# Kernel optimization log

Measured on AMD Instinct MI355X. Metric: run time of the kernel, lower is better.

The kernel has to match this reference:

```python
import jax, jax.numpy as jnp
import numpy as np

HIDDEN = 2048
N_HEADS = 16
HEAD_DIM = 128
N_KV_HEADS = 4
MAX_POS = 4096
NEG_INF = -1e9


def _fixed_pos_embedding(features, length):
    # matches generate_fixed_pos_embedding: freqs over arange(0, features, 2)/features
    fraction = jnp.arange(0, features, 2, dtype=jnp.float32) / features
    timescale = 10000.0 ** fraction
    inv_freq = 1.0 / timescale
    sinusoid = jnp.einsum('i,j->ij', jnp.arange(length, dtype=jnp.float32), inv_freq)
    sinusoid = jnp.concatenate([sinusoid, sinusoid], axis=-1)  # [length, features]
    return jnp.sin(sinusoid), jnp.cos(sinusoid)


def setup_inputs() -> dict:
    key = jax.random.key(0)
    k0, k1, k2, k3, k4 = jax.random.split(key, 5)
    B, S = 2, 2048
    hidden_states = jax.random.normal(k0, (B, S, HIDDEN), dtype=jnp.float32)
    # causal additive mask [B,1,S,S]; module forces mask[:, :, :, 0] = 0
    causal = jnp.where(jnp.tril(jnp.ones((S, S), dtype=bool)), 0.0, NEG_INF).astype(jnp.float32)
    causal = causal.at[:, 0].set(0.0)
    attention_mask = jnp.broadcast_to(causal[None, None], (B, 1, S, S))
    std = 0.02
    q_w = jax.random.normal(k1, (N_HEADS * HEAD_DIM, HIDDEN), dtype=jnp.float32) * std
    k_w = jax.random.normal(k2, (N_KV_HEADS * HEAD_DIM, HIDDEN), dtype=jnp.float32) * std
    v_w = jax.random.normal(k3, (N_KV_HEADS * HEAD_DIM, HIDDEN), dtype=jnp.float32) * std
    o_w = jax.random.normal(k4, (HIDDEN, N_HEADS * HEAD_DIM), dtype=jnp.float32) * std
    sin, cos = _fixed_pos_embedding(HEAD_DIM, MAX_POS)
    return {"hidden_states": hidden_states, "attention_mask": attention_mask,
            "q_w": q_w, "k_w": k_w, "v_w": v_w, "o_w": o_w, "sin": sin, "cos": cos}


def _rotate_half(x):
    d = x.shape[-1] // 2
    return jnp.concatenate([-x[..., d:], x[..., :d]], axis=-1)


def reference(hidden_states, attention_mask, q_w, k_w, v_w, o_w, sin, cos):
    B, S, _ = hidden_states.shape
    D = cos.shape[-1]
    H = q_w.shape[0] // D
    KV = k_w.shape[0] // D
    n_rep = H // KV

    # QKV projections (nn.Linear: y = x @ W^T), split into heads: [B,S,h,D]
    q = jnp.einsum('bsh,oh->bso', hidden_states, q_w).reshape(B, S, H, D)
    k = jnp.einsum('bsh,oh->bso', hidden_states, k_w).reshape(B, S, KV, D)
    v = jnp.einsum('bsh,oh->bso', hidden_states, v_w).reshape(B, S, KV, D)

    # rotary embedding (non-decode path: q and k share cos/sin[:S])
    c = cos[:S][None, :, None, :]
    s = sin[:S][None, :, None, :]
    q = q * c + _rotate_half(q) * s
    k = k * c + _rotate_half(k) * s

    # repeat_kv (repeat_interleave along head dim) for GQA
    k = jnp.repeat(k, n_rep, axis=2)  # [B,S,H,D]
    v = jnp.repeat(v, n_rep, axis=2)

    # NOTE: no 1/sqrt(D) scaling -- module uses softmax_scale=1.0
    scores = jnp.einsum('bqhd,bkhd->bhqk', q, k) + attention_mask
    weights = jax.nn.softmax(scores.astype(jnp.float32), axis=-1).astype(q.dtype)
    attn = jnp.einsum('bhqk,bkhd->bqhd', weights, v).reshape(B, S, H * D)
    return jnp.einsum('bso,ho->bsh', attn, o_w)
```

## Files before the change

### kernel.cpp

```cpp
#include <hip/hip_runtime.h>

typedef __bf16 bf16x8 __attribute__((ext_vector_type(8)));
typedef float f32x4 __attribute__((ext_vector_type(4)));

#define LOG2E 1.44269504088896340736f

#define GLDS16(g, l) __builtin_amdgcn_global_load_lds(                         \
    (const __attribute__((address_space(1))) unsigned int*)(g),                \
    (__attribute__((address_space(3))) unsigned int*)(l), 16, 0, 0)


__global__ __launch_bounds__(256) void megasplit(
    const float* __restrict__ hs, const float* __restrict__ qw,
    const float* __restrict__ kw, const float* __restrict__ vw,
    const float* __restrict__ ow,
    __bf16* __restrict__ hsh, __bf16* __restrict__ hsl,
    __bf16* __restrict__ wqh, __bf16* __restrict__ wql,
    __bf16* __restrict__ owh, __bf16* __restrict__ owl)
{
    int bid = blockIdx.x;
    const float* src; __bf16* dh; __bf16* dl;
    if (bid < 4096)      { src = hs; dh = hsh; dl = hsl; }
    else if (bid < 6144) { bid -= 4096; src = qw; dh = wqh; dl = wql; }
    else if (bid < 6656) { bid -= 6144; src = kw;
                           dh = wqh + (size_t)2048 * 2048;
                           dl = wql + (size_t)2048 * 2048; }
    else if (bid < 7168) { bid -= 6656; src = vw;
                           dh = wqh + (size_t)2560 * 2048;
                           dl = wql + (size_t)2560 * 2048; }
    else                 { bid -= 7168; src = ow; dh = owh; dl = owl; }

    const size_t t = (size_t)(bid * 256 + threadIdx.x) * 8;
    float4 a = *(const float4*)(src + t);
    float4 b = *(const float4*)(src + t + 4);
    float f[8] = {a.x, a.y, a.z, a.w, b.x, b.y, b.z, b.w};
    bf16x8 h, l;
#pragma unroll
    for (int i = 0; i < 8; ++i) {
        __bf16 hh = (__bf16)f[i];
        h[i] = hh; l[i] = (__bf16)(f[i] - (float)hh);
    }
    const int r  = (int)(t >> 11);
    const int sw = (r ^ (r >> 2)) & 3;
    const size_t d = (t & ~(size_t)31) + ((size_t)((((int)(t >> 3) & 3) ^ sw)) << 3);
    *(bf16x8*)(dh + d) = h;
    *(bf16x8*)(dl + d) = l;
}

template<int BN, int NLOAD>
__global__ __launch_bounds__(512, 2) void gemm_planes8(
    const __bf16* __restrict__ Ah, const __bf16* __restrict__ Al,
    const __bf16* __restrict__ Bh, const __bf16* __restrict__ Bl,
    float* __restrict__ C, int ldc)
{
    constexpr int WN = BN / 4;
    constexpr int NF = WN / 16;

    __shared__ __bf16 sAh[2][256 * 32];
    __shared__ __bf16 sAl[2][256 * 32];
    __shared__ __bf16 sBh[2][BN * 32];
    __shared__ __bf16 sBl[2][BN * 32];

    const int tid  = threadIdx.x;
    const int lane = tid & 63;
    const int wave = tid >> 6;
    const int wm   = (wave & 1) * 128;
    const int wn   = (wave >> 1) * WN;

    const int idg = blockIdx.y * 16 + blockIdx.x;
    const int swb = (idg & 7) * 32 + (idg >> 3);
    const int m0  = (swb >> 4) * 256;
    const int n0  = (swb & 15) * BN;

    const int fr  = lane & 15;
    const int g   = lane >> 4;
    const int dr  = g * 4;
    const int sxr = (fr ^ (fr >> 2)) & 3;
    const int pA  = (g ^ sxr) << 3;

    const int srow = tid >> 2;
    const int spb  = (tid & 3) << 3;
    const __bf16* gAh0 = Ah + (size_t)(m0 + srow) * 2048 + spb;
    const __bf16* gAh1 = gAh0 + (size_t)128 * 2048;
    const __bf16* gAl0 = Al + (size_t)(m0 + srow) * 2048 + spb;
    const __bf16* gAl1 = gAl0 + (size_t)128 * 2048;
    const __bf16* gBh0 = Bh + (size_t)(n0 + srow) * 2048 + spb;
    const __bf16* gBl0 = Bl + (size_t)(n0 + srow) * 2048 + spb;
    const __bf16* gX5  = Bl;
    const __bf16* gBl6 = Bl;
    if constexpr (BN == 192) {
        gX5 = (tid < 256)
            ? Bh + (size_t)(n0 + 128 + srow) * 2048 + spb
            : Bl + (size_t)(n0 + ((tid - 256) >> 2)) * 2048 + (((tid - 256) & 3) << 3);
        gBl6 = Bl + (size_t)(n0 + 64 + srow) * 2048 + spb;
    }

#define STAGE8(bb)                                                             \
    do {                                                                       \
        GLDS16(gAh0, &sAh[bb][tid * 8]);                                       \
        GLDS16(gAh1, &sAh[bb][4096 + tid * 8]);                                \
        GLDS16(gAl0, &sAl[bb][tid * 8]);                                       \
        GLDS16(gAl1, &sAl[bb][4096 + tid * 8]);                                \
        GLDS16(gBh0, &sBh[bb][tid * 8]);                                       \
        if constexpr (BN == 192) {                                             \
            if (tid < 256) { GLDS16(gX5, &sBh[bb][4096 + tid * 8]); }          \
            else           { GLDS16(gX5, &sBl[bb][(tid - 256) * 8]); }         \
            GLDS16(gBl6, &sBl[bb][2048 + tid * 8]);                            \
        } else {                                                               \
            GLDS16(gBl0, &sBl[bb][tid * 8]);                                   \
        }                                                                      \
    } while (0)

#define ADV8()                                                                 \
    do {                                                                       \
        gAh0 += 32; gAh1 += 32; gAl0 += 32; gAl1 += 32;                        \
        gBh0 += 32; gBl0 += 32;                                                \
        if constexpr (BN == 192) { gX5 += 32; gBl6 += 32; }                    \
    } while (0)

    f32x4 acc[8][NF];
#pragma unroll
    for (int mf = 0; mf < 8; ++mf)
#pragma unroll
        for (int nf = 0; nf < NF; ++nf)
            acc[mf][nf] = (f32x4){0.f, 0.f, 0.f, 0.f};

    STAGE8(0);
    ADV8();

    for (int t = 0; t < 64; ++t) {
        const int buf = t & 1;

        __builtin_amdgcn_sched_barrier(0);
        asm volatile("s_waitcnt vmcnt(0)" ::: "memory");
        __builtin_amdgcn_sched_barrier(0);
        __builtin_amdgcn_s_barrier();
        __builtin_amdgcn_sched_barrier(0);
        if (t < 63) {
            STAGE8(buf ^ 1);
            ADV8();
        }
        __builtin_amdgcn_sched_barrier(0);

        bf16x8 bh[NF], bl[NF];
#pragma unroll
        for (int nf = 0; nf < NF; ++nf) {
            bh[nf] = *(const bf16x8*)&sBh[buf][(wn + nf * 16 + fr) * 32 + pA];
            bl[nf] = *(const bf16x8*)&sBl[buf][(wn + nf * 16 + fr) * 32 + pA];
        }
        __builtin_amdgcn_s_setprio(1);
#pragma unroll
        for (int p = 0; p < 4; ++p) {
            bf16x8 a0h = *(const bf16x8*)&sAh[buf][(wm + p * 32 + fr) * 32 + pA];
            bf16x8 a0l = *(const bf16x8*)&sAl[buf][(wm + p * 32 + fr) * 32 + pA];
            bf16x8 a1h = *(const bf16x8*)&sAh[buf][(wm + p * 32 + 16 + fr) * 32 + pA];
            bf16x8 a1l = *(const bf16x8*)&sAl[buf][(wm + p * 32 + 16 + fr) * 32 + pA];
#pragma unroll
            for (int nf = 0; nf < NF; ++nf) {
                acc[2 * p][nf] = __builtin_amdgcn_mfma_f32_16x16x32_bf16(a0h, bh[nf], acc[2 * p][nf], 0, 0, 0);
                acc[2 * p][nf] = __builtin_amdgcn_mfma_f32_16x16x32_bf16(a0l, bh[nf], acc[2 * p][nf], 0, 0, 0);
                acc[2 * p][nf] = __builtin_amdgcn_mfma_f32_16x16x32_bf16(a0h, bl[nf], acc[2 * p][nf], 0, 0, 0);
                acc[2 * p + 1][nf] = __builtin_amdgcn_mfma_f32_16x16x32_bf16(a1h, bh[nf], acc[2 * p + 1][nf], 0, 0, 0);
                acc[2 * p + 1][nf] = __builtin_amdgcn_mfma_f32_16x16x32_bf16(a1l, bh[nf], acc[2 * p + 1][nf], 0, 0, 0);
                acc[2 * p + 1][nf] = __builtin_amdgcn_mfma_f32_16x16x32_bf16(a1h, bl[nf], acc[2 * p + 1][nf], 0, 0, 0);
            }
        }
        __builtin_amdgcn_s_setprio(0);
    }

#pragma unroll
    for (int mf = 0; mf < 8; ++mf)
#pragma unroll
        for (int nf = 0; nf < NF; ++nf)
#pragma unroll
            for (int rr = 0; rr < 4; ++rr) {
                const int row = m0 + wm + mf * 16 + dr + rr;
                const int col = n0 + wn + nf * 16 + fr;
                C[(size_t)row * ldc + col] = acc[mf][nf][rr];
            }
#undef STAGE8
#undef ADV8
}

__global__ __launch_bounds__(256) void rope_prep(
    float* __restrict__ qkv,
    const float* __restrict__ sinp, const float* __restrict__ cosp,
    __bf16* __restrict__ ksp, __bf16* __restrict__ vtsp)
{
    __shared__ float vs[32][132];
    const int tid = threadIdx.x;

    if (blockIdx.x < 16384) {
        int t = blockIdx.x * 256 + tid;
        int row = t >> 10;
        int rem = t & 1023;
        int col = (rem >> 6) * 128 + (rem & 63);
        int s = row & 2047;
        int d = col & 127;

        float* p = qkv + (size_t)row * 3072 + col;
        float x0  = p[0];
        float x1  = p[64];
        float c0  = cosp[s * 128 + d];
        float c1  = cosp[s * 128 + d + 64];
        float sn0 = sinp[s * 128 + d];
        float sn1 = sinp[s * 128 + d + 64];
        p[0]  = x0 * c0 - x1 * sn0;
        p[64] = x1 * c1 + x0 * sn1;
        return;
    }

    const int pidx = blockIdx.x - 16384;
    const int kb  = pidx & 15;
    const int kvh = (pidx >> 4) & 3;
    const int b   = pidx >> 6;

    {
        const int key = tid >> 1;
        const int dh  = (tid & 1) * 32;
        const int pos = kb * 128 + key;
        const int ksw = key & 7;
        const float* src = qkv + (size_t)(b * 2048 + pos) * 3072 + 2048 + kvh * 128;
        __bf16* dst = ksp + ((size_t)((b * 4 + kvh) * 2048) + pos) * 256;
        const float* cp = cosp + pos * 128;
        const float* sp = sinp + pos * 128;
#pragma unroll
        for (int g = 0; g < 4; ++g) {
            int d0 = dh + g * 8;
            float4 x0a = *(const float4*)(src + d0);
            float4 x0b = *(const float4*)(src + d0 + 4);
            float4 x1a = *(const float4*)(src + d0 + 64);
            float4 x1b = *(const float4*)(src + d0 + 68);
            float4 c0a = *(const float4*)(cp + d0);
            float4 c0b = *(const float4*)(cp + d0 + 4);
            float4 c1a = *(const float4*)(cp + d0 + 64);
            float4 c1b = *(const float4*)(cp + d0 + 68);
            float4 s0a = *(const float4*)(sp + d0);
            float4 s0b = *(const float4*)(sp + d0 + 4);
            float4 s1a = *(const float4*)(sp + d0 + 64);
            float4 s1b = *(const float4*)(sp + d0 + 68);
            float x0[8] = {x0a.x,x0a.y,x0a.z,x0a.w,x0b.x,x0b.y,x0b.z,x0b.w};
            float x1[8] = {x1a.x,x1a.y,x1a.z,x1a.w,x1b.x,x1b.y,x1b.z,x1b.w};
            float c0[8] = {c0a.x,c0a.y,c0a.z,c0a.w,c0b.x,c0b.y,c0b.z,c0b.w};
            float c1[8] = {c1a.x,c1a.y,c1a.z,c1a.w,c1b.x,c1b.y,c1b.z,c1b.w};
            float s0[8] = {s0a.x,s0a.y,s0a.z,s0a.w,s0b.x,s0b.y,s0b.z,s0b.w};
            float s1[8] = {s1a.x,s1a.y,s1a.z,s1a.w,s1b.x,s1b.y,s1b.z,s1b.w};
            bf16x8 h0, l0, h1, l1;
#pragma unroll
            for (int i = 0; i < 8; ++i) {
                float y0 = x0[i] * c0[i] - x1[i] * s0[i];
                float y1 = x1[i] * c1[i] + x0[i] * s1[i];
                __bf16 hh0 = (__bf16)y0;
                __bf16 hh1 = (__bf16)y1;
                h0[i] = hh0; l0[i] = (__bf16)(y0 - (float)hh0);
                h1[i] = hh1; l1[i] = (__bf16)(y1 - (float)hh1);
            }
            const int bb = d0 >> 3;
            *(bf16x8*)(dst + ((bb        ^ ksw) << 3)) = h0;
            *(bf16x8*)(dst + (((bb + 8)  ^ ksw) << 3)) = h1;
            *(bf16x8*)(dst + (((bb + 16) ^ ksw) << 3)) = l0;
            *(bf16x8*)(dst + (((bb + 24) ^ ksw) << 3)) = l1;
        }
    }

    for (int st = 0; st < 4; ++st) {
        __syncthreads();
        {
            const int key = tid >> 3;
            const int dc  = (tid & 7) * 16;
            const float* vsrc = qkv + (size_t)(b * 2048 + kb * 128 + st * 32 + key) * 3072
                                + 2560 + kvh * 128 + dc;
            float4 v0 = *(const float4*)(vsrc);
            float4 v1 = *(const float4*)(vsrc + 4);
            float4 v2 = *(const float4*)(vsrc + 8);
            float4 v3 = *(const float4*)(vsrc + 12);
            *(float4*)&vs[key][dc]      = v0;
            *(float4*)&vs[key][dc + 4]  = v1;
            *(float4*)&vs[key][dc + 8]  = v2;
            *(float4*)&vs[key][dc + 12] = v3;
        }
        __syncthreads();
        {
            const int plane = tid >> 7;
            const int d     = tid & 127;
            bf16x8 ob[4];
#pragma unroll
            for (int k = 0; k < 32; ++k) {
                float x = vs[k][d];
                __bf16 hh = (__bf16)x;
                ob[k >> 3][k & 7] = plane ? (__bf16)(x - (float)hh) : hh;
            }
            const int rV  = plane * 128 + d;
            const int vsw = (d >> 1) & 3;
            __bf16* dst = vtsp + ((size_t)((b * 4 + kvh) * 64 + kb * 4 + st)) * 8192
                               + (size_t)rV * 32;
            *(bf16x8*)(dst + ((0 ^ vsw) << 3)) = ob[0];
            *(bf16x8*)(dst + ((1 ^ vsw) << 3)) = ob[1];
            *(bf16x8*)(dst + ((2 ^ vsw) << 3)) = ob[2];
            *(bf16x8*)(dst + ((3 ^ vsw) << 3)) = ob[3];
        }
    }
}

__global__ __launch_bounds__(512, 4) void flash_attn(
    const float* __restrict__ qkv,
    const __bf16* __restrict__ ksp,
    const __bf16* __restrict__ vtsp,
    __bf16* __restrict__ attnh, __bf16* __restrict__ attnl)
{
    __shared__ __bf16 Ks[2][32 * 256];
    __shared__ __bf16 Vt[2][256 * 32];
    __shared__ unsigned int Psf[4][2][512];

    const int tid  = threadIdx.x;
    const int lane = tid & 63;
    const int wave = tid >> 6;
    const int hw   = wave & 3;
    const int rs   = wave >> 2;
    const int id   = blockIdx.x;
    const int pair = id & 7;
    const int kvh  = pair & 3;
    const int b    = pair >> 2;
    const int u    = id >> 3;
    const int qb   = (u >> 5) ? (u & 31) : 63 - (u & 31);
    const int h    = kvh * 4 + hw;

    const int fr  = lane & 15;
    const int g   = lane >> 4;
    const int fc  = g * 8;
    const int dr  = g * 4;
    const int frs = fr & 7;

    bf16x8 aqh[4], aql[4];
    {
        const size_t qrow = (size_t)(b * 2048 + qb * 32 + rs * 16 + fr) * 3072 + h * 128;
#pragma unroll
        for (int ks = 0; ks < 4; ++ks) {
            float4 qv[2];
            qv[0] = *(const float4*)(qkv + qrow + ks * 32 + fc);
            qv[1] = *(const float4*)(qkv + qrow + ks * 32 + fc + 4);
            const float* qf = (const float*)qv;
            bf16x8 h8, l8;
#pragma unroll
            for (int i = 0; i < 8; ++i) {
                float x = qf[i];
                __bf16 hh = (__bf16)x;
                h8[i] = hh; l8[i] = (__bf16)(x - (float)hh);
            }
            aqh[ks] = h8; aql[ks] = l8;
        }
    }
    asm volatile("s_waitcnt vmcnt(0)" ::: "memory");
    __builtin_amdgcn_sched_barrier(0);

    bf16x8 ones;
#pragma unroll
    for (int i = 0; i < 8; ++i) ones[i] = (__bf16)1.0f;

    f32x4 o[8];
#pragma unroll
    for (int dg = 0; dg < 8; ++dg) o[dg] = (f32x4){0.f, 0.f, 0.f, 0.f};
    f32x4 ls = (f32x4){0.f, 0.f, 0.f, 0.f};

    const int ntiles = qb + 1;
    const __bf16* kg0 = ksp + (size_t)(b * 4 + kvh) * 2048 * 256 + wave * 1024 + lane * 8;
    const __bf16* vg0 = vtsp + (size_t)(b * 4 + kvh) * 64 * 8192 + wave * 1024 + lane * 8;

    {
        __bf16* kl = &Ks[0][wave * 1024];
        __bf16* vl = &Vt[0][wave * 1024];
        GLDS16(kg0, kl); GLDS16(kg0 + 512, kl + 512);
        GLDS16(vg0, vl); GLDS16(vg0 + 512, vl + 512);
    }

    for (int kt = 0; kt < ntiles; ++kt) {
        if (kt + 1 < ntiles) {
            const __bf16* kg = kg0 + (size_t)(kt + 1) * 8192;
            const __bf16* vg = vg0 + (size_t)(kt + 1) * 8192;
            __bf16* kl = &Ks[(kt + 1) & 1][wave * 1024];
            __bf16* vl = &Vt[(kt + 1) & 1][wave * 1024];
            GLDS16(kg, kl); GLDS16(kg + 512, kl + 512);
            GLDS16(vg, vl); GLDS16(vg + 512, vl + 512);
            asm volatile("s_waitcnt vmcnt(4)" ::: "memory");
        } else {
            asm volatile("s_waitcnt vmcnt(0)" ::: "memory");
        }
        __builtin_amdgcn_sched_barrier(0);
        __builtin_amdgcn_s_barrier();
        __builtin_amdgcn_sched_barrier(0);

        const int buf = kt & 1;
        const int k0 = kt * 32;

        f32x4 s0v = (f32x4){0.f, 0.f, 0.f, 0.f};
        f32x4 s1v = (f32x4){0.f, 0.f, 0.f, 0.f};
        __builtin_amdgcn_s_setprio(1);
#pragma unroll
        for (int ks = 0; ks < 4; ++ks) {
            const int bh = ks * 4 + g;
            bf16x8 b0h = *(const bf16x8*)&Ks[buf][fr * 256        + ((bh        ^ frs) << 3)];
            bf16x8 b0l = *(const bf16x8*)&Ks[buf][fr * 256        + (((bh + 16) ^ frs) << 3)];
            bf16x8 b1h = *(const bf16x8*)&Ks[buf][(16 + fr) * 256 + ((bh        ^ frs) << 3)];
            bf16x8 b1l = *(const bf16x8*)&Ks[buf][(16 + fr) * 256 + (((bh + 16) ^ frs) << 3)];
            s0v = __builtin_amdgcn_mfma_f32_16x16x32_bf16(aqh[ks], b0h, s0v, 0, 0, 0);
            s0v = __builtin_amdgcn_mfma_f32_16x16x32_bf16(aql[ks], b0h, s0v, 0, 0, 0);
            s0v = __builtin_amdgcn_mfma_f32_16x16x32_bf16(aqh[ks], b0l, s0v, 0, 0, 0);
            s1v = __builtin_amdgcn_mfma_f32_16x16x32_bf16(aqh[ks], b1h, s1v, 0, 0, 0);
            s1v = __builtin_amdgcn_mfma_f32_16x16x32_bf16(aql[ks], b1h, s1v, 0, 0, 0);
            s1v = __builtin_amdgcn_mfma_f32_16x16x32_bf16(aqh[ks], b1l, s1v, 0, 0, 0);
        }
        __builtin_amdgcn_s_setprio(0);

        if (kt == ntiles - 1) {
#pragma unroll
            for (int r = 0; r < 4; ++r) {
                const int qg = qb * 32 + rs * 16 + dr + r;
                if (k0 + fr > qg)      s0v[r] = -1e30f;
                if (k0 + 16 + fr > qg) s1v[r] = -1e30f;
            }
        }
        {
            uint4 w0, w1;
#pragma unroll
            for (int r = 0; r < 4; ++r) {
                float x0 = exp2f(s0v[r] * LOG2E);
                float x1 = exp2f(s1v[r] * LOG2E);
                __bf16 h0 = (__bf16)x0;
                __bf16 h1 = (__bf16)x1;
                unsigned u0 = ((unsigned)__builtin_bit_cast(unsigned short, h0) << 16)
                            |  (unsigned)__builtin_bit_cast(unsigned short, (__bf16)(x0 - (float)h0));
                unsigned u1 = ((unsigned)__builtin_bit_cast(unsigned short, h1) << 16)
                            |  (unsigned)__builtin_bit_cast(unsigned short, (__bf16)(x1 - (float)h1));
                ((unsigned*)&w0)[r] = u0;
                ((unsigned*)&w1)[r] = u1;
            }
            unsigned int* pw = &Psf[hw][rs][0];
            const int sb = (fr * 4 + g) ^ (((fr >> 3) & 1) << 2);
            *(uint4*)(pw + sb * 4)        = w0;
            *(uint4*)(pw + (sb + 64) * 4) = w1;
        }
        asm volatile("s_waitcnt lgkmcnt(0)" ::: "memory");
        __builtin_amdgcn_sched_barrier(0);

        bf16x8 ph, pl;
#pragma unroll
        for (int j = 0; j < 8; ++j) {
            const int col = fc + j;
            const int sR  = (col * 4 + (fr >> 2)) ^ ((g & 1) << 2);
            const unsigned v = Psf[hw][rs][sR * 4 + (fr & 3)];
            ph[j] = __builtin_bit_cast(__bf16, (unsigned short)(v >> 16));
            pl[j] = __builtin_bit_cast(__bf16, (unsigned short)(v & 0xffffu));
        }

        __builtin_amdgcn_s_setprio(1);
        ls = __builtin_amdgcn_mfma_f32_16x16x32_bf16(ph, ones, ls, 0, 0, 0);
        ls = __builtin_amdgcn_mfma_f32_16x16x32_bf16(pl, ones, ls, 0, 0, 0);
#pragma unroll
        for (int dg = 0; dg < 8; ++dg) {
            const int d0 = dg * 16 + fr;
            const int sw = (g ^ ((d0 >> 1) & 3)) << 3;
            bf16x8 bvh = *(const bf16x8*)&Vt[buf][d0 * 32 + sw];
            bf16x8 bvl = *(const bf16x8*)&Vt[buf][(d0 + 128) * 32 + sw];
            o[dg] = __builtin_amdgcn_mfma_f32_16x16x32_bf16(ph, bvh, o[dg], 0, 0, 0);
            o[dg] = __builtin_amdgcn_mfma_f32_16x16x32_bf16(pl, bvh, o[dg], 0, 0, 0);
            o[dg] = __builtin_amdgcn_mfma_f32_16x16x32_bf16(ph, bvl, o[dg], 0, 0, 0);
        }
        __builtin_amdgcn_s_setprio(0);

        __builtin_amdgcn_s_barrier();
    }

    {
        const size_t orow = (size_t)(b * 2048 + qb * 32 + rs * 16);
#pragma unroll
        for (int dg = 0; dg < 8; ++dg)
#pragma unroll
            for (int r = 0; r < 4; ++r) {
                float val = o[dg][r] / ls[r];
                const int rl  = dr + r;
                const int swz = (rl ^ (rl >> 2)) & 3;
                const int col = h * 128 + dg * 16 + fr;
                const size_t idx = (size_t)(orow + rl) * 2048 + (col & ~31)
                                 + ((((col >> 3) & 3) ^ swz) << 3) + (col & 7);
                __bf16 hh = (__bf16)val;
                attnh[idx] = hh;
                attnl[idx] = (__bf16)(val - (float)hh);
            }
    }
}

extern "C" void kernel_launch(void* const* d_in, const int* in_sizes, int n_in,
                              void* d_out, int out_size, void* d_ws, size_t ws_size,
                              hipStream_t stream)
{
    const float* hs   = (const float*)d_in[0];
    const float* qw   = (const float*)d_in[2];
    const float* kw   = (const float*)d_in[3];
    const float* vw   = (const float*)d_in[4];
    const float* ow   = (const float*)d_in[5];
    const float* sinp = (const float*)d_in[6];
    const float* cosp = (const float*)d_in[7];
    float* outp = (float*)d_out;

    char* w = (char*)d_ws;
    float*  qkv  = (float*)w;   w += (size_t)4096 * 3072 * 4;
    __bf16* ksp  = (__bf16*)w;  w += (size_t)8 * 2048 * 256 * 2;
    __bf16* vtsp = (__bf16*)w;  w += (size_t)8 * 64 * 8192 * 2;
    __bf16* wqh  = (__bf16*)w;  w += (size_t)3072 * 2048 * 2;
    __bf16* wql  = (__bf16*)w;  w += (size_t)3072 * 2048 * 2;
    __bf16* owh  = (__bf16*)w;  w += (size_t)2048 * 2048 * 2;
    __bf16* owl  = (__bf16*)w;  w += (size_t)2048 * 2048 * 2;
    __bf16* hsh  = (__bf16*)w;  w += (size_t)4096 * 2048 * 2;
    __bf16* hsl  = (__bf16*)w;  w += (size_t)4096 * 2048 * 2;
    __bf16* attnh = hsh;
    __bf16* attnl = hsl;

    megasplit<<<9216, 256, 0, stream>>>(hs, qw, kw, vw, ow,
                                        hsh, hsl, wqh, wql, owh, owl);
    gemm_planes8<192, 7><<<dim3(16, 16), 512, 0, stream>>>(hsh, hsl, wqh, wql, qkv, 3072);
    rope_prep<<<16512, 256, 0, stream>>>(qkv, sinp, cosp, ksp, vtsp);
    flash_attn<<<512, 512, 0, stream>>>(qkv, ksp, vtsp, attnh, attnl);
    gemm_planes8<128, 6><<<dim3(16, 16), 512, 0, stream>>>(attnh, attnl, owh, owl, outp, 2048);
}
```

Measured before the change: 578.5 us.

## Switch split-bf16 GEMMs to 32x32x16 MFMA with 4x2 wave tiling

Rewrites the split-precision GEMM inner loop to use 32x32x16 bf16 MFMA instructions instead of 16x16x32, and rearranges waves into a 4x2 grid of 64-row by BN/2-column tiles. Each wave now loads larger fragments per k-half and issues fewer, larger MFMAs, which is meant to cut LDS read traffic per FLOP and raise matrix-core throughput. The accumulator layout and output store indexing change to match the 32x32 fragment layout, which risks slower or less coalesced stores and higher register pressure.

```diff
diff --git a/kernel.cpp b/kernel.cpp
--- a/kernel.cpp
+++ b/kernel.cpp
@@ -2,6 +2,7 @@
 
 typedef __bf16 bf16x8 __attribute__((ext_vector_type(8)));
 typedef float f32x4 __attribute__((ext_vector_type(4)));
+typedef float f32x16 __attribute__((ext_vector_type(16)));
 
 #define LOG2E 1.44269504088896340736f
 
@@ -48,13 +49,14 @@
 }
 
 template<int BN, int NLOAD>
-__global__ __launch_bounds__(512, 2) void gemm_planes8(
+__global__ __launch_bounds__(512, 2) void gemm_planes32(
     const __bf16* __restrict__ Ah, const __bf16* __restrict__ Al,
     const __bf16* __restrict__ Bh, const __bf16* __restrict__ Bl,
     float* __restrict__ C, int ldc)
 {
-    constexpr int WN = BN / 4;
-    constexpr int NF = WN / 16;
+    constexpr int WN = BN / 2;
+    constexpr int CF = WN / 32;
+    constexpr int RF = 2;
 
     __shared__ __bf16 sAh[2][256 * 32];
     __shared__ __bf16 sAl[2][256 * 32];
@@ -64,19 +66,17 @@
     const int tid  = threadIdx.x;
     const int lane = tid & 63;
     const int wave = tid >> 6;
-    const int wm   = (wave & 1) * 128;
-    const int wn   = (wave >> 1) * WN;
+    const int wmr  = (wave & 3) * 64;
+    const int wnc  = (wave >> 2) * WN;
 
     const int idg = blockIdx.y * 16 + blockIdx.x;
     const int swb = (idg & 7) * 32 + (idg >> 3);
     const int m0  = (swb >> 4) * 256;
     const int n0  = (swb & 15) * BN;
 
-    const int fr  = lane & 15;
-    const int g   = lane >> 4;
-    const int dr  = g * 4;
-    const int sxr = (fr ^ (fr >> 2)) & 3;
-    const int pA  = (g ^ sxr) << 3;
+    const int rl  = lane & 31;
+    const int kh  = lane >> 5;
+    const int srl = (rl ^ (rl >> 2)) & 3;
 
     const int srow = tid >> 2;
     const int spb  = (tid & 3) << 3;
@@ -118,12 +118,12 @@
         if constexpr (BN == 192) { gX5 += 32; gBl6 += 32; }                    \
     } while (0)
 
-    f32x4 acc[8][NF];
-#pragma unroll
-    for (int mf = 0; mf < 8; ++mf)
-#pragma unroll
-        for (int nf = 0; nf < NF; ++nf)
-            acc[mf][nf] = (f32x4){0.f, 0.f, 0.f, 0.f};
+    f32x16 acc[RF][CF];
+#pragma unroll
+    for (int rf = 0; rf < RF; ++rf)
+#pragma unroll
+        for (int cf = 0; cf < CF; ++cf)
+            acc[rf][cf] = (f32x16){0.f};
 
     STAGE8(0);
     ADV8();
@@ -142,41 +142,49 @@
         }
         __builtin_amdgcn_sched_barrier(0);
 
-        bf16x8 bh[NF], bl[NF];
-#pragma unroll
-        for (int nf = 0; nf < NF; ++nf) {
-            bh[nf] = *(const bf16x8*)&sBh[buf][(wn + nf * 16 + fr) * 32 + pA];
-            bl[nf] = *(const bf16x8*)&sBl[buf][(wn + nf * 16 + fr) * 32 + pA];
-        }
         __builtin_amdgcn_s_setprio(1);
 #pragma unroll
-        for (int p = 0; p < 4; ++p) {
-            bf16x8 a0h = *(const bf16x8*)&sAh[buf][(wm + p * 32 + fr) * 32 + pA];
-            bf16x8 a0l = *(const bf16x8*)&sAl[buf][(wm + p * 32 + fr) * 32 + pA];
-            bf16x8 a1h = *(const bf16x8*)&sAh[buf][(wm + p * 32 + 16 + fr) * 32 + pA];
-            bf16x8 a1l = *(const bf16x8*)&sAl[buf][(wm + p * 32 + 16 + fr) * 32 + pA];
-#pragma unroll
-            for (int nf = 0; nf < NF; ++nf) {
-                acc[2 * p][nf] = __builtin_amdgcn_mfma_f32_16x16x32_bf16(a0h, bh[nf], acc[2 * p][nf], 0, 0, 0);
-                acc[2 * p][nf] = __builtin_amdgcn_mfma_f32_16x16x32_bf16(a0l, bh[nf], acc[2 * p][nf], 0, 0, 0);
-                acc[2 * p][nf] = __builtin_amdgcn_mfma_f32_16x16x32_bf16(a0h, bl[nf], acc[2 * p][nf], 0, 0, 0);
-                acc[2 * p + 1][nf] = __builtin_amdgcn_mfma_f32_16x16x32_bf16(a1h, bh[nf], acc[2 * p + 1][nf], 0, 0, 0);
-                acc[2 * p + 1][nf] = __builtin_amdgcn_mfma_f32_16x16x32_bf16(a1l, bh[nf], acc[2 * p + 1][nf], 0, 0, 0);
-                acc[2 * p + 1][nf] = __builtin_amdgcn_mfma_f32_16x16x32_bf16(a1h, bl[nf], acc[2 * p + 1][nf], 0, 0, 0);
-            }
+        for (int kk = 0; kk < 2; ++kk) {
+            bf16x8 ah[RF], al[RF], bhf[CF], blf[CF];
+#pragma unroll
+            for (int rf = 0; rf < RF; ++rf) {
+                const int ra = (wmr + rf * 32 + rl) * 32
+                             + (((kk * 2 + kh) ^ srl) << 3);
+                ah[rf] = *(const bf16x8*)&sAh[buf][ra];
+                al[rf] = *(const bf16x8*)&sAl[buf][ra];
+            }
+#pragma unroll
+            for (int cf = 0; cf < CF; ++cf) {
+                const int rb = (wnc + cf * 32 + rl) * 32
+                             + (((kk * 2 + kh) ^ srl) << 3);
+                bhf[cf] = *(const bf16x8*)&sBh[buf][rb];
+                blf[cf] = *(const bf16x8*)&sBl[buf][rb];
+            }
+#pragma unroll
+            for (int rf = 0; rf < RF; ++rf)
+#pragma unroll
+                for (int cf = 0; cf < CF; ++cf) {
+                    acc[rf][cf] = __builtin_amdgcn_mfma_f32_32x32x16_bf16(
+                        ah[rf], bhf[cf], acc[rf][cf], 0, 0, 0);
+                    acc[rf][cf] = __builtin_amdgcn_mfma_f32_32x32x16_bf16(
+                        al[rf], bhf[cf], acc[rf][cf], 0, 0, 0);
+                    acc[rf][cf] = __builtin_amdgcn_mfma_f32_32x32x16_bf16(
+                        ah[rf], blf[cf], acc[rf][cf], 0, 0, 0);
+                }
         }
         __builtin_amdgcn_s_setprio(0);
     }
 
 #pragma unroll
-    for (int mf = 0; mf < 8; ++mf)
-#pragma unroll
-        for (int nf = 0; nf < NF; ++nf)
-#pragma unroll
-            for (int rr = 0; rr < 4; ++rr) {
-                const int row = m0 + wm + mf * 16 + dr + rr;
-                const int col = n0 + wn + nf * 16 + fr;
-                C[(size_t)row * ldc + col] = acc[mf][nf][rr];
+    for (int rf = 0; rf < RF; ++rf)
+#pragma unroll
+        for (int cf = 0; cf < CF; ++cf)
+#pragma unroll
+            for (int reg = 0; reg < 16; ++reg) {
+                const int row = m0 + wmr + rf * 32
+                              + (reg & 3) + 8 * (reg >> 2) + 4 * kh;
+                const int col = n0 + wnc + cf * 32 + rl;
+                C[(size_t)row * ldc + col] = acc[rf][cf][reg];
             }
 #undef STAGE8
 #undef ADV8
@@ -517,8 +525,8 @@
 
     megasplit<<<9216, 256, 0, stream>>>(hs, qw, kw, vw, ow,
                                         hsh, hsl, wqh, wql, owh, owl);
-    gemm_planes8<192, 7><<<dim3(16, 16), 512, 0, stream>>>(hsh, hsl, wqh, wql, qkv, 3072);
+    gemm_planes32<192, 7><<<dim3(16, 16), 512, 0, stream>>>(hsh, hsl, wqh, wql, qkv, 3072);
     rope_prep<<<16512, 256, 0, stream>>>(qkv, sinp, cosp, ksp, vtsp);
     flash_attn<<<512, 512, 0, stream>>>(qkv, ksp, vtsp, attnh, attnl);
-    gemm_planes8<128, 6><<<dim3(16, 16), 512, 0, stream>>>(attnh, attnl, owh, owl, outp, 2048);
+    gemm_planes32<128, 6><<<dim3(16, 16), 512, 0, stream>>>(attnh, attnl, owh, owl, outp, 2048);
 }
```

Result: no change. 570.8 us (-1.3%).
